# Kernel tuning notes

Hardware: AMD Instinct MI355X
Metric: run time of the kernel (lower is better)

The kernel has to match this reference:

```python
import jax, jax.numpy as jnp
import numpy as np

N, E, H, IN = 4096, 65536, 256, 16
N_BLOCKS, N_SUB = 3, 2
IE = 2 * H + 2  # edge-mlp input: h[row] ++ h[col] ++ edge_attr(2)
NORM_FACTOR = 100.0


def setup_inputs() -> dict:
    key = jax.random.key(0)
    ks = jax.random.split(key, 24)
    G = N_BLOCKS * N_SUB  # 6 GCLs total

    def p(k, shape, fan_in, gain=1.0):
        return gain * jax.random.normal(k, shape, jnp.float32) / np.sqrt(fan_in)

    return {
        "h": jax.random.normal(ks[0], (N, IN), jnp.float32),
        "x": jax.random.normal(ks[1], (N, 3), jnp.float32),
        "edge_index": jax.random.randint(ks[2], (2, E), 0, N),
        # embedding in/out
        "emb_w": p(ks[3], (IN, H), IN), "emb_b": jnp.zeros((H,), jnp.float32),
        "out_w": p(ks[4], (H, IN), H), "out_b": jnp.zeros((IN,), jnp.float32),
        # GCL edge MLP (stacked over the 6 GCLs)
        "edge_w1": p(ks[5], (G, IE, H), IE), "edge_b1": jnp.zeros((G, H), jnp.float32),
        "edge_w2": p(ks[6], (G, H, H), H), "edge_b2": jnp.zeros((G, H), jnp.float32),
        # GCL node MLP
        "node_w1": p(ks[7], (G, 2 * H, H), 2 * H), "node_b1": jnp.zeros((G, H), jnp.float32),
        "node_w2": p(ks[8], (G, H, H), H), "node_b2": jnp.zeros((G, H), jnp.float32),
        # EquivariantUpdate coord MLP (stacked over 3 blocks); last layer xavier gain=0.001, no bias
        "coord_w1": p(ks[9], (N_BLOCKS, IE, H), IE), "coord_b1": jnp.zeros((N_BLOCKS, H), jnp.float32),
        "coord_w2": p(ks[10], (N_BLOCKS, H, H), H), "coord_b2": jnp.zeros((N_BLOCKS, H), jnp.float32),
        "coord_w3": p(ks[11], (N_BLOCKS, H, 1), H, gain=0.001),
    }


def reference(h, x, edge_index, emb_w, emb_b, out_w, out_b,
              edge_w1, edge_b1, edge_w2, edge_b2,
              node_w1, node_b1, node_w2, node_b2,
              coord_w1, coord_b1, coord_w2, coord_b2, coord_w3):
    row, col = edge_index[0], edge_index[1]
    n_nodes = h.shape[0]

    def seg_sum(data):  # unsorted_segment_sum with 'sum' aggregation / normalization_factor
        return jax.ops.segment_sum(data, row, num_segments=n_nodes) / NORM_FACTOR

    def coord2diff(xc):  # norm_constant = 1
        d = xc[row] - xc[col]                      # [E,3]
        radial = jnp.sum(d * d, axis=1, keepdims=True)  # [E,1]
        cd = d / (jnp.sqrt(radial + 1e-8) + 1.0)
        return radial, cd

    dist0, _ = coord2diff(x)          # EGNN-level distances (from initial coords)
    h = h @ emb_w + emb_b             # node embedding

    gi = 0
    for b in range(N_BLOCKS):
        radial, coord_diff = coord2diff(x)
        ea = jnp.concatenate([radial, dist0], axis=1)   # [E,2] edge_attr
        for _ in range(N_SUB):  # GCL sublayers
            m = jnp.concatenate([h[row], h[col], ea], axis=1)           # [E, 2H+2]
            m = jax.nn.silu(m @ edge_w1[gi] + edge_b1[gi])
            m = jax.nn.silu(m @ edge_w2[gi] + edge_b2[gi])              # [E, H]
            agg = seg_sum(m)                                            # [N, H]
            u = jnp.concatenate([h, agg], axis=1)                       # [N, 2H]
            u = jax.nn.silu(u @ node_w1[gi] + node_b1[gi])
            h = h + u @ node_w2[gi] + node_b2[gi]                       # residual node update
            gi += 1
        # EquivariantUpdate (tanh=False)
        t = jnp.concatenate([h[row], h[col], ea], axis=1)
        t = jax.nn.silu(t @ coord_w1[b] + coord_b1[b])
        t = jax.nn.silu(t @ coord_w2[b] + coord_b2[b])
        trans = coord_diff * (t @ coord_w3[b])                          # [E,3]
        x = x + seg_sum(trans)

    h = h @ out_w + out_b
    return h, x
```

## Files before the change

kernel.cpp:

```cpp
#include <hip/hip_runtime.h>
#include <hip/hip_bf16.h>
#include <cstdint>
#include <cstddef>

#define NN 4096
#define NE 65536
#define HD 256

typedef __attribute__((ext_vector_type(4))) float f32x4;
typedef __attribute__((ext_vector_type(8))) __bf16 bf16x8;

static __device__ __forceinline__ float silu_f(float v) {
  float e = __builtin_amdgcn_exp2f(v * -1.442695040888963f);
  return v * __builtin_amdgcn_rcpf(1.f + e);
}

struct TJob { const float* src; __bf16* dst; int K; int N; };
struct TJobs { TJob j[39]; };

__global__ __launch_bounds__(256) void k_transpose(TJobs jobs) {
  TJob jb = jobs.j[blockIdx.z];
  int k0 = blockIdx.x << 5, n0 = blockIdx.y << 5;
  if (k0 >= jb.K || n0 >= jb.N) return;
  __shared__ float t[32][33];
  int tx = threadIdx.x & 31, ty = threadIdx.x >> 5;
#pragma unroll
  for (int r = ty; r < 32; r += 8)
    t[r][tx] = jb.src[(size_t)(k0 + r) * jb.N + n0 + tx];
  __syncthreads();
#pragma unroll
  for (int r = ty; r < 32; r += 8)
    jb.dst[(size_t)(n0 + r) * jb.K + k0 + tx] = (__bf16)t[tx][r];
}

__global__ __launch_bounds__(256) void k_hist(const int* __restrict__ ei, int* __restrict__ cnt) {
  int e = blockIdx.x * 256 + threadIdx.x;
  atomicAdd(&cnt[ei[e]], 1);
}

__global__ __launch_bounds__(1024) void k_scan(const int* __restrict__ cnt, int* __restrict__ offs,
                                               int* __restrict__ cursor) {
  __shared__ int tmp[1024];
  int tid = threadIdx.x;
  int v[4]; int s = 0;
#pragma unroll
  for (int i = 0; i < 4; i++) { v[i] = cnt[tid * 4 + i]; s += v[i]; }
  tmp[tid] = s;
  __syncthreads();
  for (int o = 1; o < 1024; o <<= 1) {
    int t = (tid >= o) ? tmp[tid - o] : 0;
    __syncthreads();
    tmp[tid] += t;
    __syncthreads();
  }
  int base = (tid > 0) ? tmp[tid - 1] : 0;
#pragma unroll
  for (int i = 0; i < 4; i++) {
    offs[tid * 4 + i] = base; cursor[tid * 4 + i] = base; base += v[i];
  }
  if (tid == 1023) offs[4096] = base;
}

__global__ __launch_bounds__(256) void k_scatter(const int* __restrict__ ei, int* __restrict__ cursor,
                                                 int* __restrict__ elist) {
  int e = blockIdx.x * 256 + threadIdx.x;
  int pos = atomicAdd(&cursor[ei[e]], 1);
  elist[pos] = e;
}

__global__ __launch_bounds__(256) void k_csrinit(const int* __restrict__ elist, const int* __restrict__ ei,
                                                 const float* __restrict__ x, int* __restrict__ rowp,
                                                 int* __restrict__ colp, float* __restrict__ d0p,
                                                 float* __restrict__ radp, float* __restrict__ cdp,
                                                 float* __restrict__ xc) {
  int i = blockIdx.x * 256 + threadIdx.x;
  if (i < NN * 3) xc[i] = x[i];
  int e = elist[i];
  int r = ei[e], c = ei[NE + e];
  rowp[i] = r; colp[i] = c;
  float dx = x[r * 3 + 0] - x[c * 3 + 0];
  float dy = x[r * 3 + 1] - x[c * 3 + 1];
  float dz = x[r * 3 + 2] - x[c * 3 + 2];
  float rad = dx * dx + dy * dy + dz * dz;
  d0p[i] = rad;
  radp[i] = rad;
  float inv = 1.f / (sqrtf(rad + 1e-8f) + 1.f);
  cdp[i * 3 + 0] = dx * inv; cdp[i * 3 + 1] = dy * inv; cdp[i * 3 + 2] = dz * inv;
}

__global__ __launch_bounds__(256) void k_geo(const int* __restrict__ rowp, const int* __restrict__ colp,
                                             const float* __restrict__ x, float* __restrict__ radp,
                                             float* __restrict__ cdp) {
  int i = blockIdx.x * 256 + threadIdx.x;
  int r = rowp[i], c = colp[i];
  float dx = x[r * 3 + 0] - x[c * 3 + 0];
  float dy = x[r * 3 + 1] - x[c * 3 + 1];
  float dz = x[r * 3 + 2] - x[c * 3 + 2];
  float rad = dx * dx + dy * dy + dz * dz;
  radp[i] = rad;
  float inv = 1.f / (sqrtf(rad + 1e-8f) + 1.f);
  cdp[i * 3 + 0] = dx * inv; cdp[i * 3 + 1] = dy * inv; cdp[i * 3 + 2] = dz * inv;
}

__global__ __launch_bounds__(256) void k_embed(const float* __restrict__ h0, const float* __restrict__ W,
                                               const float* __restrict__ b, float* __restrict__ hf,
                                               __bf16* __restrict__ h16) {
  int n = blockIdx.x, c = threadIdx.x;
  float s = b[c];
#pragma unroll
  for (int i = 0; i < 16; i++) s += h0[n * 16 + i] * W[i * 256 + c];
  hf[(size_t)n * HD + c] = s;
  h16[(size_t)n * HD + c] = (__bf16)s;
}

__global__ __launch_bounds__(256) void k_mkbias(const float* __restrict__ eb1, const float* __restrict__ cb1,
                                                float* __restrict__ bias512) {
  int i = blockIdx.x * 256 + threadIdx.x;
  int g = i >> 9, r = i & 511;
  float v = 0.f;
  if (r < 256) v = (g < 6) ? eb1[g * 256 + r] : cb1[(g - 6) * 256 + r];
  bias512[i] = v;
}

__global__ __launch_bounds__(256) void k_segsum(const __bf16* __restrict__ m2p, const int* __restrict__ offs,
                                                __bf16* __restrict__ agg16) {
  __shared__ float sd[8][256];
  int n = blockIdx.x, t = threadIdx.x;
  int g = t >> 5, l = t & 31;
  int c0 = l << 3;
  float a[8] = {};
  int ib = offs[n], ie = offs[n + 1];
  for (int i = ib + g; i < ie; i += 8) {
    bf16x8 v = *(const bf16x8*)(m2p + (size_t)i * 256 + c0);
#pragma unroll
    for (int j = 0; j < 8; j++) a[j] += (float)v[j];
  }
#pragma unroll
  for (int j = 0; j < 8; j++) sd[g][c0 + j] = a[j];
  __syncthreads();
  float s = 0.f;
#pragma unroll
  for (int j = 0; j < 8; j++) s += sd[j][t];
  agg16[(size_t)n * 256 + t] = (__bf16)(s * 0.01f);
}

__global__ __launch_bounds__(256) void k_xupd(const float* __restrict__ transp, const int* __restrict__ offs,
                                              float* __restrict__ xc) {
  int n = blockIdx.x * 256 + threadIdx.x;
  if (n >= NN) return;
  float a0 = 0.f, a1 = 0.f, a2 = 0.f;
  int i1 = offs[n + 1];
  for (int i = offs[n]; i < i1; i++) {
    a0 += transp[i * 3 + 0]; a1 += transp[i * 3 + 1]; a2 += transp[i * 3 + 2];
  }
  xc[n * 3 + 0] += a0 * 0.01f;
  xc[n * 3 + 1] += a1 * 0.01f;
  xc[n * 3 + 2] += a2 * 0.01f;
}

__global__ __launch_bounds__(256) void k_out(const float* __restrict__ hf, const float* __restrict__ W,
                                             const float* __restrict__ b, const float* __restrict__ xc,
                                             float* __restrict__ out) {
  int t = blockIdx.x * 256 + threadIdx.x;
  if (blockIdx.x < 256) {
    int n = t >> 4, j = t & 15;
    float s = b[j];
    for (int c = 0; c < 256; c++) s += hf[(size_t)n * HD + c] * W[c * 16 + j];
    out[n * 16 + j] = s;
  } else {
    int i = t - NN * 16;
    if (i < NN * 3) out[NN * 16 + i] = xc[i];
  }
}

template <int EPI>
__global__ __launch_bounds__(512, 4) void k_edgeblk(
    const __bf16* __restrict__ PQ, const int* __restrict__ rowp, const int* __restrict__ colp,
    const float* __restrict__ radp, const float* __restrict__ d0p,
    const float* __restrict__ w1r, const float* __restrict__ w1d,
    const __bf16* __restrict__ Bt, const float* __restrict__ b2,
    __bf16* __restrict__ m2p,
    const float* __restrict__ w3, const float* __restrict__ cdp, float* __restrict__ transp) {
  __shared__ alignas(16) char smem[37888];
  float*  wgt = (float*)smem;
  __bf16* Bs0 = (__bf16*)(smem + 4096);
  __bf16* Bs1 = (__bf16*)(smem + 4096 + 16384);
  float*  reds = (float*)(smem + 4096);

  const int tid = threadIdx.x;
  const int lane = tid & 63;
  const int w = tid >> 6;
  const int l15 = lane & 15;
  const int kg = lane >> 4;
  const int R0 = blockIdx.x * 128;
  const int rowg = R0 + w * 16 + l15;

  const __bf16* pBase = PQ + (size_t)rowp[rowg] * 512;
  const __bf16* qBase = PQ + (size_t)colp[rowg] * 512 + 256;
  const float rad = radp[rowg], dd0 = d0p[rowg];

  if (tid < 256) {
    wgt[tid]       = w1r[tid];
    wgt[256 + tid] = w1d[tid];
  } else {
    int t2 = tid - 256;
    wgt[512 + t2] = b2[t2];
    if (EPI == 1) wgt[768 + t2] = w3[t2];
  }

  int srcOff[2];
#pragma unroll
  for (int q = 0; q < 2; q++) {
    int s = q * 512 + tid;
    int n = s >> 2, g = s & 3;
    srcOff[q] = n * 256 + ((g ^ ((n >> 1) & 3)) << 3);
  }
  const int dstE0 = (0 * 512 + (w << 6)) * 8;
  const int dstE1 = (1 * 512 + (w << 6)) * 8;

  __builtin_amdgcn_global_load_lds((const unsigned int*)(Bt + srcOff[0]),
                                   (unsigned int*)(Bs0 + dstE0), 16, 0, 0);
  __builtin_amdgcn_global_load_lds((const unsigned int*)(Bt + srcOff[1]),
                                   (unsigned int*)(Bs0 + dstE1), 16, 0, 0);
  bf16x8 pvc = *(const bf16x8*)(pBase + kg * 8);
  bf16x8 qvc = *(const bf16x8*)(qBase + kg * 8);
  __syncthreads();

  f32x4 acc[16] = {};

#pragma unroll
  for (int t = 0; t < 8; t++) {
    const __bf16* Bcur = (t & 1) ? Bs1 : Bs0;
    __bf16*       Bnxt = (t & 1) ? Bs0 : Bs1;
    bf16x8 pvn, qvn;
    if (t < 7) {
      int kt = (t + 1) * 32;
      __builtin_amdgcn_global_load_lds((const unsigned int*)(Bt + kt + srcOff[0]),
                                       (unsigned int*)(Bnxt + dstE0), 16, 0, 0);
      __builtin_amdgcn_global_load_lds((const unsigned int*)(Bt + kt + srcOff[1]),
                                       (unsigned int*)(Bnxt + dstE1), 16, 0, 0);
      __builtin_amdgcn_sched_barrier(0);
      pvn = *(const bf16x8*)(pBase + kt + kg * 8);
      qvn = *(const bf16x8*)(qBase + kt + kg * 8);
    }
    const int k0 = t * 32 + kg * 8;
    f32x4 wr0 = *(const f32x4*)&wgt[k0],       wr1 = *(const f32x4*)&wgt[k0 + 4];
    f32x4 wd0 = *(const f32x4*)&wgt[256 + k0], wd1 = *(const f32x4*)&wgt[256 + k0 + 4];
    bf16x8 af;
#pragma unroll
    for (int j = 0; j < 4; j++)
      af[j] = (__bf16)silu_f((float)pvc[j] + (float)qvc[j] + rad * wr0[j] + dd0 * wd0[j]);
#pragma unroll
    for (int j = 0; j < 4; j++)
      af[4 + j] = (__bf16)silu_f((float)pvc[4 + j] + (float)qvc[4 + j] + rad * wr1[j] + dd0 * wd1[j]);
    __builtin_amdgcn_s_setprio(1);
#pragma unroll
    for (int fn = 0; fn < 16; fn++) {
      int n = fn * 16 + l15;
      bf16x8 bf = *(const bf16x8*)&Bcur[n * 32 + ((kg ^ ((n >> 1) & 3)) << 3)];
      acc[fn] = __builtin_amdgcn_mfma_f32_16x16x32_bf16(af, bf, acc[fn], 0, 0, 0);
    }
    __builtin_amdgcn_s_setprio(0);
    if (t < 7) { pvc = pvn; qvc = qvn; }
    __builtin_amdgcn_sched_barrier(0);
    asm volatile("s_waitcnt vmcnt(2) lgkmcnt(0)" ::: "memory");
    __builtin_amdgcn_s_barrier();
    __builtin_amdgcn_sched_barrier(0);
  }

  if (EPI == 0) {
    __bf16* ep = (__bf16*)(smem + 4096 + w * 4224);
#pragma unroll
    for (int p = 0; p < 2; p++) {
      if ((kg >> 1) == p) {
        int rl = (kg & 1) * 4;
#pragma unroll
        for (int fn = 0; fn < 16; fn++) {
          int col = fn * 16 + l15;
          float bv = wgt[512 + col];
#pragma unroll
          for (int j = 0; j < 4; j++)
            ep[(rl + j) * 264 + col] = (__bf16)silu_f(acc[fn][j] + bv);
        }
      }
      __syncthreads();
#pragma unroll
      for (int i = 0; i < 4; i++) {
        int r = i * 2 + (lane >> 5);
        int g = lane & 31;
        uint4 v = *(const uint4*)&ep[r * 264 + g * 8];
        *(uint4*)(m2p + ((size_t)(R0 + w * 16 + p * 8 + r)) * 256 + g * 8) = v;
      }
      __syncthreads();
    }
  } else {
    float s[4] = {0.f, 0.f, 0.f, 0.f};
#pragma unroll
    for (int fn = 0; fn < 16; fn++) {
      int col = fn * 16 + l15;
      float bv = wgt[512 + col], wv = wgt[768 + col];
#pragma unroll
      for (int j = 0; j < 4; j++)
        s[j] += silu_f(acc[fn][j] + bv) * wv;
    }
#pragma unroll
    for (int off = 1; off < 16; off <<= 1)
#pragma unroll
      for (int j = 0; j < 4; j++)
        s[j] += __shfl_xor(s[j], off, 64);
    __syncthreads();
    if (l15 == 0) {
#pragma unroll
      for (int j = 0; j < 4; j++)
        reds[w * 16 + kg * 4 + j] = s[j];
    }
    __syncthreads();
    if (tid < 128) {
      float sv = reds[tid];
      size_t i = (size_t)R0 + tid;
      transp[i * 3 + 0] = cdp[i * 3 + 0] * sv;
      transp[i * 3 + 1] = cdp[i * 3 + 1] * sv;
      transp[i * 3 + 2] = cdp[i * 3 + 2] * sv;
    }
  }
}

template <int EPI, int SPLIT>
__global__ __launch_bounds__(256) void k_gemm64(const __bf16* __restrict__ A, const __bf16* __restrict__ A2,
                                                const __bf16* __restrict__ Bt,
                                                const float* __restrict__ bias, __bf16* __restrict__ outb,
                                                float* __restrict__ outf, int M, int N, int K) {
  constexpr int BM = 64, BN = 64, BK = 64;
  __shared__ __bf16 As[2][BM * BK];
  __shared__ __bf16 Bs[2][BN * BK];
  const int tid = threadIdx.x;
  const int lane = tid & 63;
  const int wave = tid >> 6;
  const int wm = wave >> 1, wn = wave & 1;
  const size_t m0 = (size_t)blockIdx.x * BM;
  const size_t n0 = (size_t)blockIdx.y * BN;
  const int r0 = tid >> 3, g0 = tid & 7;
  const int gs0 = (g0 ^ (r0 & 7)) << 3;
  const int Astride = SPLIT ? 256 : K;

  f32x4 acc[2][2] = {};
  const int NT = K >> 6;

  {
    uint4 a0 = *(const uint4*)(A + (m0 + r0) * Astride + g0 * 8);
    uint4 a1 = *(const uint4*)(A + (m0 + r0 + 32) * Astride + g0 * 8);
    uint4 b0 = *(const uint4*)(Bt + (n0 + r0) * K + g0 * 8);
    uint4 b1 = *(const uint4*)(Bt + (n0 + r0 + 32) * K + g0 * 8);
    *(uint4*)&As[0][r0 * BK + gs0] = a0;
    *(uint4*)&As[0][(r0 + 32) * BK + gs0] = a1;
    *(uint4*)&Bs[0][r0 * BK + gs0] = b0;
    *(uint4*)&Bs[0][(r0 + 32) * BK + gs0] = b1;
  }
  __syncthreads();

  int buf = 0;
  for (int t = 0; t < NT; ++t) {
    const bool has = (t + 1 < NT);
    uint4 a0, a1, b0, b1;
    if (has) {
      int kt = (t + 1) << 6;
      const __bf16* Ab;
      int ko;
      if (SPLIT) { Ab = (kt < 256) ? A : A2; ko = kt & 255; }
      else       { Ab = A; ko = kt; }
      a0 = *(const uint4*)(Ab + (m0 + r0) * Astride + ko + g0 * 8);
      a1 = *(const uint4*)(Ab + (m0 + r0 + 32) * Astride + ko + g0 * 8);
      b0 = *(const uint4*)(Bt + (n0 + r0) * K + kt + g0 * 8);
      b1 = *(const uint4*)(Bt + (n0 + r0 + 32) * K + kt + g0 * 8);
    }
#pragma unroll
    for (int ks = 0; ks < BK; ks += 32) {
      const int kg = (ks >> 3) + (lane >> 4);
      bf16x8 af[2], bfv[2];
#pragma unroll
      for (int fm = 0; fm < 2; fm++) {
        int r = wm * 32 + fm * 16 + (lane & 15);
        af[fm] = *(const bf16x8*)&As[buf][r * BK + ((kg ^ (r & 7)) << 3)];
      }
#pragma unroll
      for (int fn = 0; fn < 2; fn++) {
        int r = wn * 32 + fn * 16 + (lane & 15);
        bfv[fn] = *(const bf16x8*)&Bs[buf][r * BK + ((kg ^ (r & 7)) << 3)];
      }
#pragma unroll
      for (int fm = 0; fm < 2; fm++)
#pragma unroll
        for (int fn = 0; fn < 2; fn++)
          acc[fm][fn] = __builtin_amdgcn_mfma_f32_16x16x32_bf16(af[fm], bfv[fn], acc[fm][fn], 0, 0, 0);
    }
    if (has) {
      *(uint4*)&As[buf ^ 1][r0 * BK + gs0] = a0;
      *(uint4*)&As[buf ^ 1][(r0 + 32) * BK + gs0] = a1;
      *(uint4*)&Bs[buf ^ 1][r0 * BK + gs0] = b0;
      *(uint4*)&Bs[buf ^ 1][(r0 + 32) * BK + gs0] = b1;
    }
    __syncthreads();
    buf ^= 1;
  }

#pragma unroll
  for (int fm = 0; fm < 2; fm++) {
#pragma unroll
    for (int fn = 0; fn < 2; fn++) {
      const size_t col = n0 + wn * 32 + fn * 16 + (lane & 15);
      float bv = bias[col];
#pragma unroll
      for (int j = 0; j < 4; j++) {
        size_t row = m0 + wm * 32 + fm * 16 + ((lane >> 4) << 2) + j;
        size_t idx = row * (size_t)N + col;
        float v = acc[fm][fn][j] + bv;
        if (EPI == 1) {
          outb[idx] = (__bf16)silu_f(v);
        } else if (EPI == 2) {
          float nh = outf[idx] + v;
          outf[idx] = nh;
          outb[idx] = (__bf16)nh;
        } else {
          outb[idx] = (__bf16)v;
        }
      }
    }
  }
}

extern "C" void kernel_launch(void* const* d_in, const int* in_sizes, int n_in,
                              void* d_out, int out_size, void* d_ws, size_t ws_size,
                              hipStream_t stream) {
  const float* h_in    = (const float*)d_in[0];
  const float* x_in    = (const float*)d_in[1];
  const int*   ei      = (const int*)d_in[2];
  const float* emb_w   = (const float*)d_in[3];
  const float* emb_b   = (const float*)d_in[4];
  const float* out_w   = (const float*)d_in[5];
  const float* out_b   = (const float*)d_in[6];
  const float* edge_w1 = (const float*)d_in[7];
  const float* edge_b1 = (const float*)d_in[8];
  const float* edge_w2 = (const float*)d_in[9];
  const float* edge_b2 = (const float*)d_in[10];
  const float* node_w1 = (const float*)d_in[11];
  const float* node_b1 = (const float*)d_in[12];
  const float* node_w2 = (const float*)d_in[13];
  const float* node_b2 = (const float*)d_in[14];
  const float* coord_w1 = (const float*)d_in[15];
  const float* coord_b1 = (const float*)d_in[16];
  const float* coord_w2 = (const float*)d_in[17];
  const float* coord_b2 = (const float*)d_in[18];
  const float* coord_w3 = (const float*)d_in[19];

  char* p = (char*)d_ws;
  auto alloc = [&](size_t bytes) -> void* {
    void* r = (void*)p;
    p += (bytes + 255) & ~(size_t)255;
    return r;
  };
  __bf16* e1T  = (__bf16*)alloc((size_t)6 * 512 * 256 * 2);
  __bf16* e2T  = (__bf16*)alloc((size_t)6 * 256 * 256 * 2);
  __bf16* n1T  = (__bf16*)alloc((size_t)6 * 256 * 512 * 2);
  __bf16* n2T  = (__bf16*)alloc((size_t)6 * 256 * 256 * 2);
  __bf16* c1T  = (__bf16*)alloc((size_t)3 * 512 * 256 * 2);
  __bf16* c2T  = (__bf16*)alloc((size_t)3 * 256 * 256 * 2);
  __bf16* h16  = (__bf16*)alloc((size_t)NN * HD * 2);
  __bf16* PQ16 = (__bf16*)alloc((size_t)NN * 512 * 2);
  __bf16* m2p  = (__bf16*)alloc((size_t)NE * HD * 2);
  __bf16* agg16 = (__bf16*)alloc((size_t)NN * HD * 2);
  __bf16* u    = (__bf16*)alloc((size_t)NN * HD * 2);
  float* hf    = (float*)alloc((size_t)NN * HD * 4);
  float* xc    = (float*)alloc((size_t)NN * 3 * 4);
  float* d0p   = (float*)alloc((size_t)NE * 4);
  float* radp  = (float*)alloc((size_t)NE * 4);
  float* cdp   = (float*)alloc((size_t)NE * 3 * 4);
  float* transp = (float*)alloc((size_t)NE * 3 * 4);
  float* bias512 = (float*)alloc((size_t)9 * 512 * 4);
  int* cnt     = (int*)alloc((size_t)NN * 4);
  int* offs    = (int*)alloc((size_t)(NN + 1) * 4);
  int* cursor  = (int*)alloc((size_t)NN * 4);
  int* elist   = (int*)alloc((size_t)NE * 4);
  int* rowp    = (int*)alloc((size_t)NE * 4);
  int* colp    = (int*)alloc((size_t)NE * 4);

  TJobs jobs;
  int nj = 0;
  for (int gi = 0; gi < 6; gi++) {
    jobs.j[nj++] = { edge_w1 + (size_t)gi * 514 * 256,             e1T + (size_t)gi * 512 * 256,             256, 256 };
    jobs.j[nj++] = { edge_w1 + (size_t)gi * 514 * 256 + 256 * 256, e1T + (size_t)gi * 512 * 256 + 256 * 256, 256, 256 };
    jobs.j[nj++] = { edge_w2 + (size_t)gi * 256 * 256,             e2T + (size_t)gi * 256 * 256,             256, 256 };
    jobs.j[nj++] = { node_w1 + (size_t)gi * 512 * 256,             n1T + (size_t)gi * 256 * 512,             512, 256 };
    jobs.j[nj++] = { node_w2 + (size_t)gi * 256 * 256,             n2T + (size_t)gi * 256 * 256,             256, 256 };
  }
  for (int b = 0; b < 3; b++) {
    jobs.j[nj++] = { coord_w1 + (size_t)b * 514 * 256,             c1T + (size_t)b * 512 * 256,              256, 256 };
    jobs.j[nj++] = { coord_w1 + (size_t)b * 514 * 256 + 256 * 256, c1T + (size_t)b * 512 * 256 + 256 * 256,  256, 256 };
    jobs.j[nj++] = { coord_w2 + (size_t)b * 256 * 256,             c2T + (size_t)b * 256 * 256,              256, 256 };
  }

  hipMemsetAsync(cnt, 0, (size_t)NN * 4, stream);
  k_transpose<<<dim3(16, 8, 39), 256, 0, stream>>>(jobs);
  k_hist<<<NE / 256, 256, 0, stream>>>(ei, cnt);
  k_scan<<<1, 1024, 0, stream>>>(cnt, offs, cursor);
  k_scatter<<<NE / 256, 256, 0, stream>>>(ei, cursor, elist);
  k_csrinit<<<NE / 256, 256, 0, stream>>>(elist, ei, x_in, rowp, colp, d0p, radp, cdp, xc);
  k_mkbias<<<18, 256, 0, stream>>>(edge_b1, coord_b1, bias512);
  k_embed<<<NN, 256, 0, stream>>>(h_in, emb_w, emb_b, hf, h16);

  int gi = 0;
  for (int b = 0; b < 3; b++) {
    for (int s = 0; s < 2; s++, gi++) {
      const float* w1 = edge_w1 + (size_t)gi * 514 * 256;
      k_gemm64<5, 0><<<dim3(64, 8), 256, 0, stream>>>(
          h16, nullptr, e1T + (size_t)gi * 512 * 256, bias512 + gi * 512, PQ16, nullptr, NN, 512, 256);
      k_edgeblk<0><<<NE / 128, 512, 0, stream>>>(
          PQ16, rowp, colp, radp, d0p, w1 + 512 * 256, w1 + 513 * 256,
          e2T + (size_t)gi * 256 * 256, edge_b2 + gi * 256, m2p, nullptr, nullptr, nullptr);
      k_segsum<<<NN, 256, 0, stream>>>(m2p, offs, agg16);
      k_gemm64<1, 1><<<dim3(64, 4), 256, 0, stream>>>(
          h16, agg16, n1T + (size_t)gi * 256 * 512, node_b1 + gi * 256, u, nullptr, NN, 256, 512);
      k_gemm64<2, 0><<<dim3(64, 4), 256, 0, stream>>>(
          u, nullptr, n2T + (size_t)gi * 256 * 256, node_b2 + gi * 256, h16, hf, NN, 256, 256);
    }
    const float* w1c = coord_w1 + (size_t)b * 514 * 256;
    k_gemm64<5, 0><<<dim3(64, 8), 256, 0, stream>>>(
        h16, nullptr, c1T + (size_t)b * 512 * 256, bias512 + (6 + b) * 512, PQ16, nullptr, NN, 512, 256);
    k_edgeblk<1><<<NE / 128, 512, 0, stream>>>(
        PQ16, rowp, colp, radp, d0p, w1c + 512 * 256, w1c + 513 * 256,
        c2T + (size_t)b * 256 * 256, coord_b2 + b * 256, nullptr,
        coord_w3 + (size_t)b * 256, cdp, transp);
    k_xupd<<<NN / 256, 256, 0, stream>>>(transp, offs, xc);
    if (b < 2) k_geo<<<NE / 256, 256, 0, stream>>>(rowp, colp, xc, radp, cdp);
  }
  k_out<<<256 + 48, 256, 0, stream>>>(hf, out_w, out_b, xc, (float*)d_out);
}
```

Before: 463.5 us.

## Double edge-block tile to 256 edges with 1024 threads and K-step 64

```diff
diff --git a/kernel.cpp b/kernel.cpp
--- a/kernel.cpp
+++ b/kernel.cpp
@@ -174,17 +174,17 @@
 }
 
 template <int EPI>
-__global__ __launch_bounds__(512, 4) void k_edgeblk(
+__global__ __launch_bounds__(1024, 4) void k_edgeblk(
     const __bf16* __restrict__ PQ, const int* __restrict__ rowp, const int* __restrict__ colp,
     const float* __restrict__ radp, const float* __restrict__ d0p,
     const float* __restrict__ w1r, const float* __restrict__ w1d,
     const __bf16* __restrict__ Bt, const float* __restrict__ b2,
     __bf16* __restrict__ m2p,
     const float* __restrict__ w3, const float* __restrict__ cdp, float* __restrict__ transp) {
-  __shared__ alignas(16) char smem[37888];
+  __shared__ alignas(16) char smem[69632];
   float*  wgt = (float*)smem;
   __bf16* Bs0 = (__bf16*)(smem + 4096);
-  __bf16* Bs1 = (__bf16*)(smem + 4096 + 16384);
+  __bf16* Bs1 = (__bf16*)(smem + 4096 + 32768);
   float*  reds = (float*)(smem + 4096);
 
   const int tid = threadIdx.x;
@@ -192,84 +192,90 @@
   const int w = tid >> 6;
   const int l15 = lane & 15;
   const int kg = lane >> 4;
-  const int R0 = blockIdx.x * 128;
+  const int R0 = blockIdx.x * 256;
   const int rowg = R0 + w * 16 + l15;
 
   const __bf16* pBase = PQ + (size_t)rowp[rowg] * 512;
   const __bf16* qBase = PQ + (size_t)colp[rowg] * 512 + 256;
   const float rad = radp[rowg], dd0 = d0p[rowg];
 
-  if (tid < 256) {
-    wgt[tid]       = w1r[tid];
-    wgt[256 + tid] = w1d[tid];
-  } else {
-    int t2 = tid - 256;
-    wgt[512 + t2] = b2[t2];
-    if (EPI == 1) wgt[768 + t2] = w3[t2];
-  }
-
+  {
+    int sel = tid >> 8, t2 = tid & 255;
+    if (sel == 0)      wgt[t2] = w1r[t2];
+    else if (sel == 1) wgt[256 + t2] = w1d[t2];
+    else if (sel == 2) wgt[512 + t2] = b2[t2];
+    else if (EPI == 1) wgt[768 + t2] = w3[t2];
+  }
+
+  const int n_ = tid >> 2, g_ = tid & 3;
   int srcOff[2];
 #pragma unroll
-  for (int q = 0; q < 2; q++) {
-    int s = q * 512 + tid;
-    int n = s >> 2, g = s & 3;
-    srcOff[q] = n * 256 + ((g ^ ((n >> 1) & 3)) << 3);
-  }
-  const int dstE0 = (0 * 512 + (w << 6)) * 8;
-  const int dstE1 = (1 * 512 + (w << 6)) * 8;
+  for (int q = 0; q < 2; q++)
+    srcOff[q] = n_ * 256 + q * 32 + ((g_ ^ ((n_ >> 1) & 3)) << 3);
+  const int dstE0 = (0 * 1024 + (w << 6)) * 8;
+  const int dstE1 = (1 * 1024 + (w << 6)) * 8;
 
   __builtin_amdgcn_global_load_lds((const unsigned int*)(Bt + srcOff[0]),
                                    (unsigned int*)(Bs0 + dstE0), 16, 0, 0);
   __builtin_amdgcn_global_load_lds((const unsigned int*)(Bt + srcOff[1]),
                                    (unsigned int*)(Bs0 + dstE1), 16, 0, 0);
-  bf16x8 pvc = *(const bf16x8*)(pBase + kg * 8);
-  bf16x8 qvc = *(const bf16x8*)(qBase + kg * 8);
+  bf16x8 p0c = *(const bf16x8*)(pBase + kg * 8);
+  bf16x8 p1c = *(const bf16x8*)(pBase + 32 + kg * 8);
+  bf16x8 q0c = *(const bf16x8*)(qBase + kg * 8);
+  bf16x8 q1c = *(const bf16x8*)(qBase + 32 + kg * 8);
   __syncthreads();
 
   f32x4 acc[16] = {};
 
 #pragma unroll
-  for (int t = 0; t < 8; t++) {
+  for (int t = 0; t < 4; t++) {
     const __bf16* Bcur = (t & 1) ? Bs1 : Bs0;
     __bf16*       Bnxt = (t & 1) ? Bs0 : Bs1;
-    bf16x8 pvn, qvn;
-    if (t < 7) {
-      int kt = (t + 1) * 32;
+    bf16x8 p0n, p1n, q0n, q1n;
+    if (t < 3) {
+      int kt = (t + 1) * 64;
       __builtin_amdgcn_global_load_lds((const unsigned int*)(Bt + kt + srcOff[0]),
                                        (unsigned int*)(Bnxt + dstE0), 16, 0, 0);
       __builtin_amdgcn_global_load_lds((const unsigned int*)(Bt + kt + srcOff[1]),
                                        (unsigned int*)(Bnxt + dstE1), 16, 0, 0);
       __builtin_amdgcn_sched_barrier(0);
-      pvn = *(const bf16x8*)(pBase + kt + kg * 8);
-      qvn = *(const bf16x8*)(qBase + kt + kg * 8);
-    }
-    const int k0 = t * 32 + kg * 8;
-    f32x4 wr0 = *(const f32x4*)&wgt[k0],       wr1 = *(const f32x4*)&wgt[k0 + 4];
-    f32x4 wd0 = *(const f32x4*)&wgt[256 + k0], wd1 = *(const f32x4*)&wgt[256 + k0 + 4];
-    bf16x8 af;
-#pragma unroll
-    for (int j = 0; j < 4; j++)
-      af[j] = (__bf16)silu_f((float)pvc[j] + (float)qvc[j] + rad * wr0[j] + dd0 * wd0[j]);
-#pragma unroll
-    for (int j = 0; j < 4; j++)
-      af[4 + j] = (__bf16)silu_f((float)pvc[4 + j] + (float)qvc[4 + j] + rad * wr1[j] + dd0 * wd1[j]);
-    __builtin_amdgcn_s_setprio(1);
-#pragma unroll
-    for (int fn = 0; fn < 16; fn++) {
-      int n = fn * 16 + l15;
-      bf16x8 bf = *(const bf16x8*)&Bcur[n * 32 + ((kg ^ ((n >> 1) & 3)) << 3)];
-      acc[fn] = __builtin_amdgcn_mfma_f32_16x16x32_bf16(af, bf, acc[fn], 0, 0, 0);
-    }
-    __builtin_amdgcn_s_setprio(0);
-    if (t < 7) { pvc = pvn; qvc = qvn; }
+      p0n = *(const bf16x8*)(pBase + kt + kg * 8);
+      p1n = *(const bf16x8*)(pBase + kt + 32 + kg * 8);
+      q0n = *(const bf16x8*)(qBase + kt + kg * 8);
+      q1n = *(const bf16x8*)(qBase + kt + 32 + kg * 8);
+    }
+#pragma unroll
+    for (int ks = 0; ks < 2; ks++) {
+      const int k0 = t * 64 + ks * 32 + kg * 8;
+      f32x4 wr0 = *(const f32x4*)&wgt[k0],       wr1 = *(const f32x4*)&wgt[k0 + 4];
+      f32x4 wd0 = *(const f32x4*)&wgt[256 + k0], wd1 = *(const f32x4*)&wgt[256 + k0 + 4];
+      bf16x8 pv = ks ? p1c : p0c;
+      bf16x8 qv = ks ? q1c : q0c;
+      bf16x8 af;
+#pragma unroll
+      for (int j = 0; j < 4; j++)
+        af[j] = (__bf16)silu_f((float)pv[j] + (float)qv[j] + rad * wr0[j] + dd0 * wd0[j]);
+#pragma unroll
+      for (int j = 0; j < 4; j++)
+        af[4 + j] = (__bf16)silu_f((float)pv[4 + j] + (float)qv[4 + j] + rad * wr1[j] + dd0 * wd1[j]);
+      __builtin_amdgcn_s_setprio(1);
+#pragma unroll
+      for (int fn = 0; fn < 16; fn++) {
+        int n = fn * 16 + l15;
+        bf16x8 bf = *(const bf16x8*)&Bcur[ks * 8192 + n * 32 + ((kg ^ ((n >> 1) & 3)) << 3)];
+        acc[fn] = __builtin_amdgcn_mfma_f32_16x16x32_bf16(af, bf, acc[fn], 0, 0, 0);
+      }
+      __builtin_amdgcn_s_setprio(0);
+    }
+    if (t < 3) { p0c = p0n; p1c = p1n; q0c = q0n; q1c = q1n; }
     __builtin_amdgcn_sched_barrier(0);
-    asm volatile("s_waitcnt vmcnt(2) lgkmcnt(0)" ::: "memory");
+    asm volatile("s_waitcnt vmcnt(4) lgkmcnt(0)" ::: "memory");
     __builtin_amdgcn_s_barrier();
     __builtin_amdgcn_sched_barrier(0);
   }
 
   if (EPI == 0) {
-    __bf16* ep = (__bf16*)(smem + 4096 + w * 4224);
+    __bf16* ep = (__bf16*)(smem + 4096) + (size_t)w * 2048;
 #pragma unroll
     for (int p = 0; p < 2; p++) {
       if ((kg >> 1) == p) {
@@ -280,7 +286,7 @@
           float bv = wgt[512 + col];
 #pragma unroll
           for (int j = 0; j < 4; j++)
-            ep[(rl + j) * 264 + col] = (__bf16)silu_f(acc[fn][j] + bv);
+            ep[(rl + j) * 256 + col] = (__bf16)silu_f(acc[fn][j] + bv);
         }
       }
       __syncthreads();
@@ -288,7 +294,7 @@
       for (int i = 0; i < 4; i++) {
         int r = i * 2 + (lane >> 5);
         int g = lane & 31;
-        uint4 v = *(const uint4*)&ep[r * 264 + g * 8];
+        uint4 v = *(const uint4*)&ep[r * 256 + g * 8];
         *(uint4*)(m2p + ((size_t)(R0 + w * 16 + p * 8 + r)) * 256 + g * 8) = v;
       }
       __syncthreads();
@@ -315,7 +321,7 @@
         reds[w * 16 + kg * 4 + j] = s[j];
     }
     __syncthreads();
-    if (tid < 128) {
+    if (tid < 256) {
       float sv = reds[tid];
       size_t i = (size_t)R0 + tid;
       transp[i * 3 + 0] = cdp[i * 3 + 0] * sv;
@@ -513,7 +519,7 @@
       const float* w1 = edge_w1 + (size_t)gi * 514 * 256;
       k_gemm64<5, 0><<<dim3(64, 8), 256, 0, stream>>>(
           h16, nullptr, e1T + (size_t)gi * 512 * 256, bias512 + gi * 512, PQ16, nullptr, NN, 512, 256);
-      k_edgeblk<0><<<NE / 128, 512, 0, stream>>>(
+      k_edgeblk<0><<<NE / 256, 1024, 0, stream>>>(
           PQ16, rowp, colp, radp, d0p, w1 + 512 * 256, w1 + 513 * 256,
           e2T + (size_t)gi * 256 * 256, edge_b2 + gi * 256, m2p, nullptr, nullptr, nullptr);
       k_segsum<<<NN, 256, 0, stream>>>(m2p, offs, agg16);
@@ -525,7 +531,7 @@
     const float* w1c = coord_w1 + (size_t)b * 514 * 256;
     k_gemm64<5, 0><<<dim3(64, 8), 256, 0, stream>>>(
         h16, nullptr, c1T + (size_t)b * 512 * 256, bias512 + (6 + b) * 512, PQ16, nullptr, NN, 512, 256);
-    k_edgeblk<1><<<NE / 128, 512, 0, stream>>>(
+    k_edgeblk<1><<<NE / 256, 1024, 0, stream>>>(
         PQ16, rowp, colp, radp, d0p, w1c + 512 * 256, w1c + 513 * 256,
         c2T + (size_t)b * 256 * 256, coord_b2 + b * 256, nullptr,
         coord_w3 + (size_t)b * 256, cdp, transp);
```

Result: slower. 485.9 us (+4.8%).

## Split fused edge MLP into elementwise layer-1 kernel and register-resident B GEMM

Applied to the files above, without the earlier changes.

```diff
diff --git a/kernel.cpp b/kernel.cpp
--- a/kernel.cpp
+++ b/kernel.cpp
@@ -173,154 +173,120 @@
   }
 }
 
-template <int EPI>
-__global__ __launch_bounds__(512, 4) void k_edgeblk(
+__global__ __launch_bounds__(256) void k_edge1(
     const __bf16* __restrict__ PQ, const int* __restrict__ rowp, const int* __restrict__ colp,
     const float* __restrict__ radp, const float* __restrict__ d0p,
     const float* __restrict__ w1r, const float* __restrict__ w1d,
-    const __bf16* __restrict__ Bt, const float* __restrict__ b2,
-    __bf16* __restrict__ m2p,
-    const float* __restrict__ w3, const float* __restrict__ cdp, float* __restrict__ transp) {
-  __shared__ alignas(16) char smem[37888];
-  float*  wgt = (float*)smem;
-  __bf16* Bs0 = (__bf16*)(smem + 4096);
-  __bf16* Bs1 = (__bf16*)(smem + 4096 + 16384);
-  float*  reds = (float*)(smem + 4096);
-
+    __bf16* __restrict__ m1p) {
+  __shared__ float wr[256], wd[256];
+  int tid = threadIdx.x;
+  wr[tid] = w1r[tid];
+  wd[tid] = w1d[tid];
+  __syncthreads();
+  int e = blockIdx.x * 32 + (tid >> 3);
+  int k0 = (tid & 7) * 32;
+  const __bf16* P = PQ + (size_t)rowp[e] * 512 + k0;
+  const __bf16* Q = PQ + (size_t)colp[e] * 512 + 256 + k0;
+  const float rad = radp[e], d0 = d0p[e];
+#pragma unroll
+  for (int q = 0; q < 4; q++) {
+    bf16x8 pv = *(const bf16x8*)(P + q * 8);
+    bf16x8 qv = *(const bf16x8*)(Q + q * 8);
+    bf16x8 o;
+#pragma unroll
+    for (int j = 0; j < 8; j++) {
+      int k = k0 + q * 8 + j;
+      o[j] = (__bf16)silu_f((float)pv[j] + (float)qv[j] + rad * wr[k] + d0 * wd[k]);
+    }
+    *(bf16x8*)(m1p + (size_t)e * 256 + k0 + q * 8) = o;
+  }
+}
+
+template <int EPI>
+__global__ __launch_bounds__(256, 2) void k_bgemm(
+    const __bf16* __restrict__ m1p, const __bf16* __restrict__ Bt,
+    const float* __restrict__ b2, const float* __restrict__ w3,
+    const float* __restrict__ cdp, __bf16* __restrict__ m2p, float* __restrict__ transp) {
+  __shared__ float sb2[256];
+  __shared__ float sw3[256];
+  __shared__ __bf16 ep[4][16 * 72];
+  __shared__ float reds[4][16];
   const int tid = threadIdx.x;
   const int lane = tid & 63;
   const int w = tid >> 6;
   const int l15 = lane & 15;
   const int kg = lane >> 4;
-  const int R0 = blockIdx.x * 128;
-  const int rowg = R0 + w * 16 + l15;
-
-  const __bf16* pBase = PQ + (size_t)rowp[rowg] * 512;
-  const __bf16* qBase = PQ + (size_t)colp[rowg] * 512 + 256;
-  const float rad = radp[rowg], dd0 = d0p[rowg];
-
-  if (tid < 256) {
-    wgt[tid]       = w1r[tid];
-    wgt[256 + tid] = w1d[tid];
-  } else {
-    int t2 = tid - 256;
-    wgt[512 + t2] = b2[t2];
-    if (EPI == 1) wgt[768 + t2] = w3[t2];
-  }
-
-  int srcOff[2];
-#pragma unroll
-  for (int q = 0; q < 2; q++) {
-    int s = q * 512 + tid;
-    int n = s >> 2, g = s & 3;
-    srcOff[q] = n * 256 + ((g ^ ((n >> 1) & 3)) << 3);
-  }
-  const int dstE0 = (0 * 512 + (w << 6)) * 8;
-  const int dstE1 = (1 * 512 + (w << 6)) * 8;
-
-  __builtin_amdgcn_global_load_lds((const unsigned int*)(Bt + srcOff[0]),
-                                   (unsigned int*)(Bs0 + dstE0), 16, 0, 0);
-  __builtin_amdgcn_global_load_lds((const unsigned int*)(Bt + srcOff[1]),
-                                   (unsigned int*)(Bs0 + dstE1), 16, 0, 0);
-  bf16x8 pvc = *(const bf16x8*)(pBase + kg * 8);
-  bf16x8 qvc = *(const bf16x8*)(qBase + kg * 8);
+  const int colbase = w * 64;
+  sb2[tid] = b2[tid];
+  if (EPI == 1) sw3[tid] = w3[tid];
   __syncthreads();
 
-  f32x4 acc[16] = {};
-
-#pragma unroll
-  for (int t = 0; t < 8; t++) {
-    const __bf16* Bcur = (t & 1) ? Bs1 : Bs0;
-    __bf16*       Bnxt = (t & 1) ? Bs0 : Bs1;
-    bf16x8 pvn, qvn;
-    if (t < 7) {
-      int kt = (t + 1) * 32;
-      __builtin_amdgcn_global_load_lds((const unsigned int*)(Bt + kt + srcOff[0]),
-                                       (unsigned int*)(Bnxt + dstE0), 16, 0, 0);
-      __builtin_amdgcn_global_load_lds((const unsigned int*)(Bt + kt + srcOff[1]),
-                                       (unsigned int*)(Bnxt + dstE1), 16, 0, 0);
-      __builtin_amdgcn_sched_barrier(0);
-      pvn = *(const bf16x8*)(pBase + kt + kg * 8);
-      qvn = *(const bf16x8*)(qBase + kt + kg * 8);
-    }
-    const int k0 = t * 32 + kg * 8;
-    f32x4 wr0 = *(const f32x4*)&wgt[k0],       wr1 = *(const f32x4*)&wgt[k0 + 4];
-    f32x4 wd0 = *(const f32x4*)&wgt[256 + k0], wd1 = *(const f32x4*)&wgt[256 + k0 + 4];
-    bf16x8 af;
-#pragma unroll
-    for (int j = 0; j < 4; j++)
-      af[j] = (__bf16)silu_f((float)pvc[j] + (float)qvc[j] + rad * wr0[j] + dd0 * wd0[j]);
-#pragma unroll
-    for (int j = 0; j < 4; j++)
-      af[4 + j] = (__bf16)silu_f((float)pvc[4 + j] + (float)qvc[4 + j] + rad * wr1[j] + dd0 * wd1[j]);
-    __builtin_amdgcn_s_setprio(1);
-#pragma unroll
-    for (int fn = 0; fn < 16; fn++) {
-      int n = fn * 16 + l15;
-      bf16x8 bf = *(const bf16x8*)&Bcur[n * 32 + ((kg ^ ((n >> 1) & 3)) << 3)];
-      acc[fn] = __builtin_amdgcn_mfma_f32_16x16x32_bf16(af, bf, acc[fn], 0, 0, 0);
-    }
-    __builtin_amdgcn_s_setprio(0);
-    if (t < 7) { pvc = pvn; qvc = qvn; }
-    __builtin_amdgcn_sched_barrier(0);
-    asm volatile("s_waitcnt vmcnt(2) lgkmcnt(0)" ::: "memory");
-    __builtin_amdgcn_s_barrier();
-    __builtin_amdgcn_sched_barrier(0);
-  }
-
-  if (EPI == 0) {
-    __bf16* ep = (__bf16*)(smem + 4096 + w * 4224);
-#pragma unroll
-    for (int p = 0; p < 2; p++) {
-      if ((kg >> 1) == p) {
-        int rl = (kg & 1) * 4;
-#pragma unroll
-        for (int fn = 0; fn < 16; fn++) {
-          int col = fn * 16 + l15;
-          float bv = wgt[512 + col];
-#pragma unroll
-          for (int j = 0; j < 4; j++)
-            ep[(rl + j) * 264 + col] = (__bf16)silu_f(acc[fn][j] + bv);
-        }
+  bf16x8 breg[4][8];
+#pragma unroll
+  for (int fn = 0; fn < 4; fn++)
+#pragma unroll
+    for (int ks = 0; ks < 8; ks++)
+      breg[fn][ks] = *(const bf16x8*)(Bt + (size_t)(colbase + fn * 16 + l15) * 256 + ks * 32 + kg * 8);
+
+  const int E0 = blockIdx.x * 128;
+  for (int c = 0; c < 8; c++) {
+    const int e0 = E0 + c * 16;
+    bf16x8 av[8];
+#pragma unroll
+    for (int ks = 0; ks < 8; ks++)
+      av[ks] = *(const bf16x8*)(m1p + (size_t)(e0 + l15) * 256 + ks * 32 + kg * 8);
+    f32x4 acc[4] = {};
+#pragma unroll
+    for (int ks = 0; ks < 8; ks++)
+#pragma unroll
+      for (int fn = 0; fn < 4; fn++)
+        acc[fn] = __builtin_amdgcn_mfma_f32_16x16x32_bf16(av[ks], breg[fn][ks], acc[fn], 0, 0, 0);
+
+    if (EPI == 0) {
+#pragma unroll
+      for (int fn = 0; fn < 4; fn++) {
+        int col = colbase + fn * 16 + l15;
+        float bv = sb2[col];
+#pragma unroll
+        for (int j = 0; j < 4; j++)
+          ep[w][(kg * 4 + j) * 72 + fn * 16 + l15] = (__bf16)silu_f(acc[fn][j] + bv);
+      }
+#pragma unroll
+      for (int p = 0; p < 2; p++) {
+        int rr = p * 8 + (lane >> 3);
+        int gg = lane & 7;
+        uint4 v = *(const uint4*)&ep[w][rr * 72 + gg * 8];
+        *(uint4*)(m2p + (size_t)(e0 + rr) * 256 + colbase + gg * 8) = v;
+      }
+    } else {
+      float s[4] = {0.f, 0.f, 0.f, 0.f};
+#pragma unroll
+      for (int fn = 0; fn < 4; fn++) {
+        int col = colbase + fn * 16 + l15;
+        float bv = sb2[col], wv = sw3[col];
+#pragma unroll
+        for (int j = 0; j < 4; j++)
+          s[j] += silu_f(acc[fn][j] + bv) * wv;
+      }
+#pragma unroll
+      for (int off = 1; off < 16; off <<= 1)
+#pragma unroll
+        for (int j = 0; j < 4; j++)
+          s[j] += __shfl_xor(s[j], off, 64);
+      if (l15 == 0) {
+#pragma unroll
+        for (int j = 0; j < 4; j++)
+          reds[w][kg * 4 + j] = s[j];
       }
       __syncthreads();
-#pragma unroll
-      for (int i = 0; i < 4; i++) {
-        int r = i * 2 + (lane >> 5);
-        int g = lane & 31;
-        uint4 v = *(const uint4*)&ep[r * 264 + g * 8];
-        *(uint4*)(m2p + ((size_t)(R0 + w * 16 + p * 8 + r)) * 256 + g * 8) = v;
+      if (tid < 16) {
+        float sv = reds[0][tid] + reds[1][tid] + reds[2][tid] + reds[3][tid];
+        size_t i = (size_t)e0 + tid;
+        transp[i * 3 + 0] = cdp[i * 3 + 0] * sv;
+        transp[i * 3 + 1] = cdp[i * 3 + 1] * sv;
+        transp[i * 3 + 2] = cdp[i * 3 + 2] * sv;
       }
       __syncthreads();
-    }
-  } else {
-    float s[4] = {0.f, 0.f, 0.f, 0.f};
-#pragma unroll
-    for (int fn = 0; fn < 16; fn++) {
-      int col = fn * 16 + l15;
-      float bv = wgt[512 + col], wv = wgt[768 + col];
-#pragma unroll
-      for (int j = 0; j < 4; j++)
-        s[j] += silu_f(acc[fn][j] + bv) * wv;
-    }
-#pragma unroll
-    for (int off = 1; off < 16; off <<= 1)
-#pragma unroll
-      for (int j = 0; j < 4; j++)
-        s[j] += __shfl_xor(s[j], off, 64);
-    __syncthreads();
-    if (l15 == 0) {
-#pragma unroll
-      for (int j = 0; j < 4; j++)
-        reds[w * 16 + kg * 4 + j] = s[j];
-    }
-    __syncthreads();
-    if (tid < 128) {
-      float sv = reds[tid];
-      size_t i = (size_t)R0 + tid;
-      transp[i * 3 + 0] = cdp[i * 3 + 0] * sv;
-      transp[i * 3 + 1] = cdp[i * 3 + 1] * sv;
-      transp[i * 3 + 2] = cdp[i * 3 + 2] * sv;
     }
   }
 }
@@ -466,6 +432,7 @@
   __bf16* c2T  = (__bf16*)alloc((size_t)3 * 256 * 256 * 2);
   __bf16* h16  = (__bf16*)alloc((size_t)NN * HD * 2);
   __bf16* PQ16 = (__bf16*)alloc((size_t)NN * 512 * 2);
+  __bf16* m1p  = (__bf16*)alloc((size_t)NE * HD * 2);
   __bf16* m2p  = (__bf16*)alloc((size_t)NE * HD * 2);
   __bf16* agg16 = (__bf16*)alloc((size_t)NN * HD * 2);
   __bf16* u    = (__bf16*)alloc((size_t)NN * HD * 2);
@@ -513,9 +480,10 @@
       const float* w1 = edge_w1 + (size_t)gi * 514 * 256;
       k_gemm64<5, 0><<<dim3(64, 8), 256, 0, stream>>>(
           h16, nullptr, e1T + (size_t)gi * 512 * 256, bias512 + gi * 512, PQ16, nullptr, NN, 512, 256);
-      k_edgeblk<0><<<NE / 128, 512, 0, stream>>>(
-          PQ16, rowp, colp, radp, d0p, w1 + 512 * 256, w1 + 513 * 256,
-          e2T + (size_t)gi * 256 * 256, edge_b2 + gi * 256, m2p, nullptr, nullptr, nullptr);
+      k_edge1<<<NE / 32, 256, 0, stream>>>(
+          PQ16, rowp, colp, radp, d0p, w1 + 512 * 256, w1 + 513 * 256, m1p);
+      k_bgemm<0><<<NE / 128, 256, 0, stream>>>(
+          m1p, e2T + (size_t)gi * 256 * 256, edge_b2 + gi * 256, nullptr, nullptr, m2p, nullptr);
       k_segsum<<<NN, 256, 0, stream>>>(m2p, offs, agg16);
       k_gemm64<1, 1><<<dim3(64, 4), 256, 0, stream>>>(
           h16, agg16, n1T + (size_t)gi * 256 * 512, node_b1 + gi * 256, u, nullptr, NN, 256, 512);
@@ -525,10 +493,11 @@
     const float* w1c = coord_w1 + (size_t)b * 514 * 256;
     k_gemm64<5, 0><<<dim3(64, 8), 256, 0, stream>>>(
         h16, nullptr, c1T + (size_t)b * 512 * 256, bias512 + (6 + b) * 512, PQ16, nullptr, NN, 512, 256);
-    k_edgeblk<1><<<NE / 128, 512, 0, stream>>>(
-        PQ16, rowp, colp, radp, d0p, w1c + 512 * 256, w1c + 513 * 256,
-        c2T + (size_t)b * 256 * 256, coord_b2 + b * 256, nullptr,
-        coord_w3 + (size_t)b * 256, cdp, transp);
+    k_edge1<<<NE / 32, 256, 0, stream>>>(
+        PQ16, rowp, colp, radp, d0p, w1c + 512 * 256, w1c + 513 * 256, m1p);
+    k_bgemm<1><<<NE / 128, 256, 0, stream>>>(
+        m1p, c2T + (size_t)b * 256 * 256, coord_b2 + b * 256, coord_w3 + (size_t)b * 256,
+        cdp, nullptr, transp);
     k_xupd<<<NN / 256, 256, 0, stream>>>(transp, offs, xc);
     if (b < 2) k_geo<<<NE / 256, 256, 0, stream>>>(rowp, colp, xc, radp, cdp);
   }
```

Result: slower. 682.4 us (+47.2%).
